# Kernel optimization log

Measured on AMD Instinct MI355X. Metric: run time of the kernel, lower is better.

Reference implementation:

```python
import jax, jax.numpy as jnp
import numpy as np

B = 524288

def setup_inputs() -> dict:
    key = jax.random.key(0)
    ks = jax.random.split(key, 9)
    return {
        "x":  jax.random.uniform(ks[0], (B, 1, 9, 9), dtype=jnp.float32),
        "Wc": jax.random.normal(ks[1], (81, 9), dtype=jnp.float32),
        "bc": jax.random.normal(ks[2], (81,), dtype=jnp.float32),
        "Wh": jax.random.normal(ks[3], (27, 9), dtype=jnp.float32),
        "bh": jax.random.normal(ks[4], (27,), dtype=jnp.float32),
        "Wm": jax.random.normal(ks[5], (12, 9), dtype=jnp.float32),
        "bm": jax.random.normal(ks[6], (12,), dtype=jnp.float32),
        "Wo": jax.random.normal(ks[7], (4, 4), dtype=jnp.float32),
        "bo": jax.random.normal(ks[8], (4,), dtype=jnp.float32),
    }

def _forward(x, Wc, bc, Wh, bh, Wm, bm, Wo, bo):
    b = x.shape[0]
    # 9 non-overlapping 3x3 patches (stride 3 over 9x9): (B, 9 patches, 9 pixels)
    p = x[:, 0].reshape(b, 3, 3, 3, 3).transpose(0, 1, 3, 2, 4).reshape(b, 9, 9)
    # conv layer: 9 logic kernels per patch -> (B, 9, 9) -> (B, 81)
    feat = jax.nn.sigmoid(
        jnp.einsum('bgp,gkp->bgk', p, Wc.reshape(9, 9, 9)) + bc.reshape(9, 9)
    ).reshape(b, 81)
    # hidden layer: 9 groups x 3 neurons, each over 9 inputs -> (B, 27)
    h = jax.nn.sigmoid(
        jnp.einsum('bgp,gnp->bgn', feat.reshape(b, 9, 9), Wh.reshape(9, 3, 9))
        + bh.reshape(9, 3)
    ).reshape(b, 27)
    # middle layer: 3 groups x 4 neurons, each over 9 inputs -> (B, 12)
    m = jax.nn.sigmoid(
        jnp.einsum('bgp,gnp->bgn', h.reshape(b, 3, 9), Wm.reshape(3, 4, 9))
        + bm.reshape(3, 4)
    ).reshape(b, 12)
    # output layer: class c reads middle group c % 3 (4 values each)
    num_classes = Wo.shape[0]
    grp = jnp.arange(num_classes) % 3                   # (C,)
    mg = m.reshape(b, 3, 4)[:, grp]                     # (B, C, 4)
    output_logits = jnp.einsum('bcp,cp->bc', mg, Wo) + bo
    return output_logits

def reference(x, Wc, bc, Wh, bh, Wm, bm, Wo, bo):
    return _forward(x, Wc, bc, Wh, bh, Wm, bm, Wo, bo)
```

## Files before the change

### kernel.cpp

```cpp
#include <hip/hip_runtime.h>

#define SAMPLES_PER_BLOCK 128
#define THREADS 128

__device__ __forceinline__ float fast_sigmoid(float v) {
    float e = __expf(-v);
    return __builtin_amdgcn_rcpf(1.0f + e);
}

__global__ __launch_bounds__(THREADS) void olcnn_kernel(
    const float* __restrict__ x,
    const float* __restrict__ Wc, const float* __restrict__ bc,
    const float* __restrict__ Wh, const float* __restrict__ bh,
    const float* __restrict__ Wm, const float* __restrict__ bm,
    const float* __restrict__ Wo, const float* __restrict__ bo,
    float* __restrict__ out)
{
    __shared__ float sx[SAMPLES_PER_BLOCK * 81];
    const int tid = threadIdx.x;
    const long long blockBase = (long long)blockIdx.x * (SAMPLES_PER_BLOCK * 81);

    const float4* xv = (const float4*)(x + blockBase);
    float4* sv = (float4*)sx;
    #pragma unroll
    for (int i = 0; i < 20; ++i)
        sv[tid + i * THREADS] = xv[tid + i * THREADS];
    if (tid < 32)
        sv[tid + 20 * THREADS] = xv[tid + 20 * THREADS];
    __syncthreads();

    const float* px = &sx[tid * 81];

    float m_out[12];
    #pragma unroll
    for (int G = 0; G < 3; ++G) {
        float hbuf[9];
        #pragma unroll
        for (int j = 0; j < 3; ++j) {
            const int g = G * 3 + j;
            const int gr = g / 3, gc = g % 3;
            float pix[9];
            #pragma unroll
            for (int pr = 0; pr < 3; ++pr)
                #pragma unroll
                for (int pc = 0; pc < 3; ++pc)
                    pix[pr * 3 + pc] = px[gr * 27 + pr * 9 + gc * 3 + pc];

            float feat[9];
            #pragma unroll
            for (int k = 0; k < 9; ++k) {
                float acc = bc[g * 9 + k];
                #pragma unroll
                for (int p = 0; p < 9; ++p)
                    acc = fmaf(pix[p], Wc[(g * 9 + k) * 9 + p], acc);
                feat[k] = fast_sigmoid(acc);
            }
            #pragma unroll
            for (int n = 0; n < 3; ++n) {
                float acc = bh[g * 3 + n];
                #pragma unroll
                for (int p = 0; p < 9; ++p)
                    acc = fmaf(feat[p], Wh[(g * 3 + n) * 9 + p], acc);
                hbuf[j * 3 + n] = fast_sigmoid(acc);
            }
        }
        #pragma unroll
        for (int n = 0; n < 4; ++n) {
            float acc = bm[G * 4 + n];
            #pragma unroll
            for (int p = 0; p < 9; ++p)
                acc = fmaf(hbuf[p], Wm[(G * 4 + n) * 9 + p], acc);
            m_out[G * 4 + n] = fast_sigmoid(acc);
        }
    }

    float res[4];
    #pragma unroll
    for (int c = 0; c < 4; ++c) {
        const int grp = c % 3;
        float acc = bo[c];
        #pragma unroll
        for (int p = 0; p < 4; ++p)
            acc = fmaf(m_out[grp * 4 + p], Wo[c * 4 + p], acc);
        res[c] = acc;
    }

    float4 o;
    o.x = res[0]; o.y = res[1]; o.z = res[2]; o.w = res[3];
    const long long sample = (long long)blockIdx.x * SAMPLES_PER_BLOCK + tid;
    ((float4*)out)[sample] = o;
}

extern "C" void kernel_launch(void* const* d_in, const int* in_sizes, int n_in,
                              void* d_out, int out_size, void* d_ws, size_t ws_size,
                              hipStream_t stream) {
    const float* x  = (const float*)d_in[0];
    const float* Wc = (const float*)d_in[1];
    const float* bc = (const float*)d_in[2];
    const float* Wh = (const float*)d_in[3];
    const float* bh = (const float*)d_in[4];
    const float* Wm = (const float*)d_in[5];
    const float* bm = (const float*)d_in[6];
    const float* Wo = (const float*)d_in[7];
    const float* bo = (const float*)d_in[8];
    float* out = (float*)d_out;

    const int B = in_sizes[0] / 81;
    const int blocks = B / SAMPLES_PER_BLOCK;
    olcnn_kernel<<<blocks, THREADS, 0, stream>>>(x, Wc, bc, Wh, bh, Wm, bm,
                                                 Wo, bo, out);
}
```

Measured before the change: 288.6 us.

## Stage input in three row-band chunks to shrink shared memory per block

Instead of copying each block's full 128x81 input tile into LDS at once, the kernel now stages one 27-float row band per sample per group G, so LDS drops to about 13.8KB per block. The output layer is folded into the G loop so the 12-element middle buffer is no longer kept live, and launch bounds request 6 blocks per SIMD. The aim is higher occupancy and lower register and LDS pressure. The cost is scalar (non-float4) global loads, 108 of 128 threads doing the staging, and extra barriers between stages that serialize load and compute.

```diff
diff --git a/kernel.cpp b/kernel.cpp
--- a/kernel.cpp
+++ b/kernel.cpp
@@ -2,13 +2,16 @@
 
 #define SAMPLES_PER_BLOCK 128
 #define THREADS 128
+#define CHUNK_FLOATS 27
+#define STAGE_THREADS 108
+#define STAGE_ITERS 32
 
 __device__ __forceinline__ float fast_sigmoid(float v) {
     float e = __expf(-v);
     return __builtin_amdgcn_rcpf(1.0f + e);
 }
 
-__global__ __launch_bounds__(THREADS) void olcnn_kernel(
+__global__ __launch_bounds__(THREADS, 6) void olcnn_kernel(
     const float* __restrict__ x,
     const float* __restrict__ Wc, const float* __restrict__ bc,
     const float* __restrict__ Wh, const float* __restrict__ bh,
@@ -16,35 +19,40 @@
     const float* __restrict__ Wo, const float* __restrict__ bo,
     float* __restrict__ out)
 {
-    __shared__ float sx[SAMPLES_PER_BLOCK * 81];
+    __shared__ float sx[SAMPLES_PER_BLOCK * CHUNK_FLOATS];
     const int tid = threadIdx.x;
-    const long long blockBase = (long long)blockIdx.x * (SAMPLES_PER_BLOCK * 81);
+    const long long sampleBase = (long long)blockIdx.x * SAMPLES_PER_BLOCK;
+    const float* xblk = x + sampleBase * 81;
 
-    const float4* xv = (const float4*)(x + blockBase);
-    float4* sv = (float4*)sx;
-    #pragma unroll
-    for (int i = 0; i < 20; ++i)
-        sv[tid + i * THREADS] = xv[tid + i * THREADS];
-    if (tid < 32)
-        sv[tid + 20 * THREADS] = xv[tid + 20 * THREADS];
-    __syncthreads();
+    const int s0 = tid / 27;
+    const int j0 = tid - s0 * 27;
 
-    const float* px = &sx[tid * 81];
+    float res[4];
 
-    float m_out[12];
     #pragma unroll
     for (int G = 0; G < 3; ++G) {
+        if (G) __syncthreads();
+        if (tid < STAGE_THREADS) {
+            const float* src = xblk + 81 * s0 + 27 * G + j0;
+            float* dst = &sx[27 * s0 + j0];
+            #pragma unroll
+            for (int i = 0; i < STAGE_ITERS; ++i)
+                dst[i * (4 * 27)] = src[i * (4 * 81)];
+        }
+        __syncthreads();
+
+        const float* px = &sx[tid * CHUNK_FLOATS];
+
         float hbuf[9];
         #pragma unroll
         for (int j = 0; j < 3; ++j) {
             const int g = G * 3 + j;
-            const int gr = g / 3, gc = g % 3;
             float pix[9];
             #pragma unroll
             for (int pr = 0; pr < 3; ++pr)
                 #pragma unroll
                 for (int pc = 0; pc < 3; ++pc)
-                    pix[pr * 3 + pc] = px[gr * 27 + pr * 9 + gc * 3 + pc];
+                    pix[pr * 3 + pc] = px[pr * 9 + j * 3 + pc];
 
             float feat[9];
             #pragma unroll
@@ -64,31 +72,36 @@
                 hbuf[j * 3 + n] = fast_sigmoid(acc);
             }
         }
+
+        float m[4];
         #pragma unroll
         for (int n = 0; n < 4; ++n) {
             float acc = bm[G * 4 + n];
             #pragma unroll
             for (int p = 0; p < 9; ++p)
                 acc = fmaf(hbuf[p], Wm[(G * 4 + n) * 9 + p], acc);
-            m_out[G * 4 + n] = fast_sigmoid(acc);
+            m[n] = fast_sigmoid(acc);
         }
-    }
 
-    float res[4];
-    #pragma unroll
-    for (int c = 0; c < 4; ++c) {
-        const int grp = c % 3;
-        float acc = bo[c];
-        #pragma unroll
-        for (int p = 0; p < 4; ++p)
-            acc = fmaf(m_out[grp * 4 + p], Wo[c * 4 + p], acc);
-        res[c] = acc;
+        {
+            float acc = bo[G];
+            #pragma unroll
+            for (int p = 0; p < 4; ++p)
+                acc = fmaf(m[p], Wo[G * 4 + p], acc);
+            res[G] = acc;
+        }
+        if (G == 0) {
+            float acc = bo[3];
+            #pragma unroll
+            for (int p = 0; p < 4; ++p)
+                acc = fmaf(m[p], Wo[3 * 4 + p], acc);
+            res[3] = acc;
+        }
     }
 
     float4 o;
     o.x = res[0]; o.y = res[1]; o.z = res[2]; o.w = res[3];
-    const long long sample = (long long)blockIdx.x * SAMPLES_PER_BLOCK + tid;
-    ((float4*)out)[sample] = o;
+    ((float4*)out)[sampleBase + tid] = o;
 }
 
 extern "C" void kernel_launch(void* const* d_in, const int* in_sizes, int n_in,
```

Result: slower. 310.1 us (+7.4%).

## Process two samples per thread with direct global loads, drop shared-memory staging

Applied to the files above, without the earlier changes.

Removes the shared-memory staging and barrier, so each thread reads its sample rows straight from global memory in three 27-float chunks. Each thread now computes two samples at once, so every uniform weight load is shared by two FMA chains, which raises instruction-level parallelism. Output-layer work is fused into the per-group loop. The cost is strided, uncoalesced global loads (81-float stride between lanes) and higher register pressure from holding 54 input floats.

```diff
diff --git a/kernel.cpp b/kernel.cpp
--- a/kernel.cpp
+++ b/kernel.cpp
@@ -1,7 +1,7 @@
 #include <hip/hip_runtime.h>
 
-#define SAMPLES_PER_BLOCK 128
-#define THREADS 128
+#define THREADS 256
+#define SAMPLES_PER_BLOCK 512
 
 __device__ __forceinline__ float fast_sigmoid(float v) {
     float e = __expf(-v);
@@ -16,79 +16,99 @@
     const float* __restrict__ Wo, const float* __restrict__ bo,
     float* __restrict__ out)
 {
-    __shared__ float sx[SAMPLES_PER_BLOCK * 81];
-    const int tid = threadIdx.x;
-    const long long blockBase = (long long)blockIdx.x * (SAMPLES_PER_BLOCK * 81);
+    const int tid  = threadIdx.x;
+    const int wave = tid >> 6, lane = tid & 63;
+    const int s0 = blockIdx.x * SAMPLES_PER_BLOCK + wave * 128 + lane;
+    const int s1 = s0 + 64;
 
-    const float4* xv = (const float4*)(x + blockBase);
-    float4* sv = (float4*)sx;
-    #pragma unroll
-    for (int i = 0; i < 20; ++i)
-        sv[tid + i * THREADS] = xv[tid + i * THREADS];
-    if (tid < 32)
-        sv[tid + 20 * THREADS] = xv[tid + 20 * THREADS];
-    __syncthreads();
+    const float* xA = x + s0 * 81;
+    const float* xB = x + s1 * 81;
 
-    const float* px = &sx[tid * 81];
+    float res[2][4];
 
-    float m_out[12];
     #pragma unroll
     for (int G = 0; G < 3; ++G) {
-        float hbuf[9];
+        float c0[27], c1[27];
+        #pragma unroll
+        for (int j = 0; j < 27; ++j) c0[j] = xA[G * 27 + j];
+        #pragma unroll
+        for (int j = 0; j < 27; ++j) c1[j] = xB[G * 27 + j];
+
+        float hb0[9], hb1[9];
         #pragma unroll
         for (int j = 0; j < 3; ++j) {
             const int g = G * 3 + j;
-            const int gr = g / 3, gc = g % 3;
-            float pix[9];
-            #pragma unroll
-            for (int pr = 0; pr < 3; ++pr)
-                #pragma unroll
-                for (int pc = 0; pc < 3; ++pc)
-                    pix[pr * 3 + pc] = px[gr * 27 + pr * 9 + gc * 3 + pc];
-
-            float feat[9];
+            float ft0[9], ft1[9];
             #pragma unroll
             for (int k = 0; k < 9; ++k) {
-                float acc = bc[g * 9 + k];
+                float a0 = bc[g * 9 + k], a1 = a0;
                 #pragma unroll
-                for (int p = 0; p < 9; ++p)
-                    acc = fmaf(pix[p], Wc[(g * 9 + k) * 9 + p], acc);
-                feat[k] = fast_sigmoid(acc);
+                for (int pr = 0; pr < 3; ++pr)
+                    #pragma unroll
+                    for (int pc = 0; pc < 3; ++pc) {
+                        const float w = Wc[(g * 9 + k) * 9 + pr * 3 + pc];
+                        const int ci = pr * 9 + j * 3 + pc;
+                        a0 = fmaf(c0[ci], w, a0);
+                        a1 = fmaf(c1[ci], w, a1);
+                    }
+                ft0[k] = fast_sigmoid(a0);
+                ft1[k] = fast_sigmoid(a1);
             }
             #pragma unroll
             for (int n = 0; n < 3; ++n) {
-                float acc = bh[g * 3 + n];
+                float a0 = bh[g * 3 + n], a1 = a0;
                 #pragma unroll
-                for (int p = 0; p < 9; ++p)
-                    acc = fmaf(feat[p], Wh[(g * 3 + n) * 9 + p], acc);
-                hbuf[j * 3 + n] = fast_sigmoid(acc);
+                for (int p = 0; p < 9; ++p) {
+                    const float w = Wh[(g * 3 + n) * 9 + p];
+                    a0 = fmaf(ft0[p], w, a0);
+                    a1 = fmaf(ft1[p], w, a1);
+                }
+                hb0[j * 3 + n] = fast_sigmoid(a0);
+                hb1[j * 3 + n] = fast_sigmoid(a1);
             }
         }
+
+        float m0[4], m1[4];
         #pragma unroll
         for (int n = 0; n < 4; ++n) {
-            float acc = bm[G * 4 + n];
+            float a0 = bm[G * 4 + n], a1 = a0;
             #pragma unroll
-            for (int p = 0; p < 9; ++p)
-                acc = fmaf(hbuf[p], Wm[(G * 4 + n) * 9 + p], acc);
-            m_out[G * 4 + n] = fast_sigmoid(acc);
+            for (int p = 0; p < 9; ++p) {
+                const float w = Wm[(G * 4 + n) * 9 + p];
+                a0 = fmaf(hb0[p], w, a0);
+                a1 = fmaf(hb1[p], w, a1);
+            }
+            m0[n] = fast_sigmoid(a0);
+            m1[n] = fast_sigmoid(a1);
+        }
+
+        {
+            float a0 = bo[G], a1 = a0;
+            #pragma unroll
+            for (int p = 0; p < 4; ++p) {
+                const float w = Wo[G * 4 + p];
+                a0 = fmaf(m0[p], w, a0);
+                a1 = fmaf(m1[p], w, a1);
+            }
+            res[0][G] = a0; res[1][G] = a1;
+        }
+        if (G == 0) {
+            float a0 = bo[3], a1 = a0;
+            #pragma unroll
+            for (int p = 0; p < 4; ++p) {
+                const float w = Wo[3 * 4 + p];
+                a0 = fmaf(m0[p], w, a0);
+                a1 = fmaf(m1[p], w, a1);
+            }
+            res[0][3] = a0; res[1][3] = a1;
         }
     }
 
-    float res[4];
-    #pragma unroll
-    for (int c = 0; c < 4; ++c) {
-        const int grp = c % 3;
-        float acc = bo[c];
-        #pragma unroll
-        for (int p = 0; p < 4; ++p)
-            acc = fmaf(m_out[grp * 4 + p], Wo[c * 4 + p], acc);
-        res[c] = acc;
-    }
-
-    float4 o;
-    o.x = res[0]; o.y = res[1]; o.z = res[2]; o.w = res[3];
-    const long long sample = (long long)blockIdx.x * SAMPLES_PER_BLOCK + tid;
-    ((float4*)out)[sample] = o;
+    float4 o0, o1;
+    o0.x = res[0][0]; o0.y = res[0][1]; o0.z = res[0][2]; o0.w = res[0][3];
+    o1.x = res[1][0]; o1.y = res[1][1]; o1.z = res[1][2]; o1.w = res[1][3];
+    ((float4*)out)[s0] = o0;
+    ((float4*)out)[s1] = o1;
 }
 
 extern "C" void kernel_launch(void* const* d_in, const int* in_sizes, int n_in,
```

After: 285.4 us. About the same (-1.1%).
